# Optimization experiments

Measured on AMD Instinct MI355X. Metric: run time of the kernel, lower is better.

Reference implementation:

```python
import jax, jax.numpy as jnp
import numpy as np

N, E, EALL, C, R = 20000, 120000, 240000, 150, 1000
EH, RH, CH = 300, 100, 150


def _seg_softmax(e, idx, n):
    m = jax.ops.segment_max(e, idx, num_segments=n)
    ex = jnp.exp(e - m[idx])
    s = jax.ops.segment_sum(ex, idx, num_segments=n)
    return ex / s[idx]


def _l2norm(x):
    return x / jnp.clip(jnp.linalg.norm(x, axis=-1, keepdims=True), 1e-12, None)


def _highway(x1, x2, w, b):
    g = jax.nn.sigmoid(x1 @ w.T + b)
    return g * x2 + (1.0 - g) * x1


def _gcn(x, ei):
    n = x.shape[0]
    j, i = ei[0], ei[1]
    deg = jax.ops.segment_sum(jnp.ones(ei.shape[1], dtype=x.dtype), i, num_segments=n)
    dis = jnp.where(deg > 0, deg ** -0.5, 0.0)
    norm = dis[j] * dis[i]
    return jax.nn.relu(jax.ops.segment_sum(norm[:, None] * x[j], i, num_segments=n))


def _gat(x, ei, ai, aj):
    n = x.shape[0]
    j, i = ei[0], ei[1]
    e = (x @ ai)[i] + (x @ aj)[j]
    alpha = _seg_softmax(jax.nn.leaky_relu(e), i, n)
    return jax.nn.relu(jax.ops.segment_sum(alpha[:, None] * x[j], i, num_segments=n))


def _gat_e(x_e, im, io, rel, triple_num, r_emb, class_index, cls_ent,
           ac, ar, wh, wt, hww, hwb, main_is_head):
    n = x_e.shape[0]
    e_cnt = im.shape[0]
    c = cls_ent.shape[0]
    x_h = jax.nn.relu(x_e @ wh.T)
    x_t = jax.nn.relu(x_e @ wt.T)
    if main_is_head:
        x_m, x_o = x_h, x_t
        v1m, v2m, v3m = ac[0], ac[1], ac[2]
        v1o, v2o, v3o = ac[4], ac[5], ac[6]
    else:
        x_m, x_o = x_t, x_h
        v1m, v2m, v3m = ac[4], ac[5], ac[6]
        v1o, v2o, v3o = ac[0], ac[1], ac[2]
    v4, acv = ac[3], ac[7]
    e1 = 0.5 * ((x_m @ v1m)[im] + (x_o @ v1o)[io]) + (r_emb @ ar[0])[rel]
    alpha = _seg_softmax(jax.nn.leaky_relu(e1), triple_num, e_cnt)
    x_edge = _l2norm(x_m[im] * alpha[:, None])  # [E, c_hidden]
    e_r = 0.5 * ((r_emb @ ar[1])[rel] + 0.5 * ((x_edge @ v3m) + (x_o @ v3o)[io]))
    e = (x_o @ v2o)[io] + e_r + (x_edge @ v2m)
    beta = _seg_softmax(jax.nn.leaky_relu(e), class_index, c)
    # literal to source: the edge-level tensor is re-indexed by node ids in spmm
    x_class = jax.ops.segment_sum(beta[:, None] * x_edge[im], class_index, num_segments=c)
    e_c = (x_class @ acv) + (x_o @ v4)[cls_ent]
    gama = _seg_softmax(jax.nn.leaky_relu(e_c), cls_ent, n)
    out = jax.ops.segment_sum(gama[:, None] * x_class, cls_ent, num_segments=n)
    return _highway(x_o, out, hww, hwb)


def _forward(x_e, r_emb_table, hw1_w, hw1_b, hw2_w, hw2_b,
             h2r_ac, h2r_ar, h2r_wh, h2r_wt, h2r_hw_w, h2r_hw_b,
             et_ac, et_ar, et_wh, et_wt, et_hw_w, et_hw_b,
             gat_ai, gat_aj,
             edge_index, rel, edge_index_all, triple_num,
             class_index_head, head_class, class_index_tail, tail_class):
    r_emb = _l2norm(r_emb_table)
    x = _highway(x_e, _gcn(x_e, edge_index_all), hw1_w, hw1_b)
    x = _highway(x, _gcn(x, edge_index_all), hw2_w, hw2_b)
    eh, et = edge_index[0], edge_index[1]
    x_e_h = _gat_e(x, et, eh, rel, triple_num, r_emb, class_index_head, head_class,
                   h2r_ac, h2r_ar, h2r_wh, h2r_wt, h2r_hw_w, h2r_hw_b, False)
    x_e_t = _gat_e(x, eh, et, rel, triple_num, r_emb, class_index_tail, tail_class,
                   et_ac, et_ar, et_wh, et_wt, et_hw_w, et_hw_b, True)
    x1 = jnp.concatenate([x, x_e_h, x_e_t], axis=1)  # [N, 600]
    return jnp.concatenate([x, _gat(x1, edge_index_all, gat_ai, gat_aj)], axis=1)  # [N, 900]


def setup_inputs() -> dict:
    key = jax.random.key(0)
    ks = jax.random.split(key, 32)
    w = lambda k, shape: (jax.random.normal(k, shape, dtype=jnp.float32) * 0.05)
    return {
        'x_e': jax.random.normal(ks[0], (N, EH), dtype=jnp.float32),
        'edge_index': jax.random.randint(ks[1], (2, E), 0, N),
        'rel': jax.random.randint(ks[2], (E,), 0, R),
        'edge_index_all': jax.random.randint(ks[3], (2, EALL), 0, N),
        'triple_num': jax.random.randint(ks[4], (E,), 0, N),
        'class_index_head': jax.random.randint(ks[5], (E,), 0, C),
        'head_class': jax.random.randint(ks[6], (C,), 0, N),
        'class_index_tail': jax.random.randint(ks[7], (E,), 0, C),
        'tail_class': jax.random.randint(ks[8], (C,), 0, N),
        'r_emb_table': jax.random.normal(ks[9], (R, RH), dtype=jnp.float32),
        'hw1_w': w(ks[10], (EH, EH)), 'hw1_b': jnp.zeros((EH,), jnp.float32),
        'hw2_w': w(ks[11], (EH, EH)), 'hw2_b': jnp.zeros((EH,), jnp.float32),
        'h2r_ac': w(ks[12], (8, CH)), 'h2r_ar': w(ks[13], (2, RH)),
        'h2r_wh': w(ks[14], (CH, EH)), 'h2r_wt': w(ks[15], (CH, EH)),
        'h2r_hw_w': w(ks[16], (CH, CH)), 'h2r_hw_b': jnp.zeros((CH,), jnp.float32),
        'et_ac': w(ks[17], (8, CH)), 'et_ar': w(ks[18], (2, RH)),
        'et_wh': w(ks[19], (CH, EH)), 'et_wt': w(ks[20], (CH, EH)),
        'et_hw_w': w(ks[21], (CH, CH)), 'et_hw_b': jnp.zeros((CH,), jnp.float32),
        'gat_ai': w(ks[22], (2 * EH,)), 'gat_aj': w(ks[23], (2 * EH,)),
    }


def reference(x_e, edge_index, rel, edge_index_all, triple_num,
              class_index_head, head_class, class_index_tail, tail_class,
              r_emb_table, hw1_w, hw1_b, hw2_w, hw2_b,
              h2r_ac, h2r_ar, h2r_wh, h2r_wt, h2r_hw_w, h2r_hw_b,
              et_ac, et_ar, et_wh, et_wt, et_hw_w, et_hw_b,
              gat_ai, gat_aj):
    return _forward(x_e, r_emb_table, hw1_w, hw1_b, hw2_w, hw2_b,
                    h2r_ac, h2r_ar, h2r_wh, h2r_wt, h2r_hw_w, h2r_hw_b,
                    et_ac, et_ar, et_wh, et_wt, et_hw_w, et_hw_b,
                    gat_ai, gat_aj,
                    edge_index, rel, edge_index_all, triple_num,
                    class_index_head, head_class, class_index_tail, tail_class)
```

## Files before the change

### kernel.cpp

```cpp
#include <hip/hip_runtime.h>
#include <math.h>

#define Nn 20000
#define Ee 120000
#define EALLe 240000
#define Cc 150
#define Rr 1000
#define EHd 300
#define RHd 100
#define CHd 150
#define CB 128
#define XSPL 16

static inline int cdiv_h(int a, int b){ return (a + b - 1) / b; }

typedef __attribute__((ext_vector_type(8))) short short8;
typedef __attribute__((ext_vector_type(4))) float f32x4;

__device__ __forceinline__ float lrelu01(float x){ return x > 0.f ? x : 0.01f * x; }

__device__ __forceinline__ unsigned short f2b(float f){
  unsigned int u = __float_as_uint(f);
  unsigned int r = (u + 0x7FFFu + ((u >> 16) & 1u)) >> 16;
  return (unsigned short)r;
}
__device__ __forceinline__ float b2f(unsigned short u){
  return __uint_as_float(((unsigned int)u) << 16);
}
__device__ __forceinline__ float b2f_lo(unsigned int u){
  return __uint_as_float(u << 16);
}
__device__ __forceinline__ float b2f_hi(unsigned int u){
  return __uint_as_float(u & 0xFFFF0000u);
}

template<int Kq>
__device__ __forceinline__ void wredsumN(float* v){
#pragma unroll
  for (int m = 32; m >= 1; m >>= 1){
#pragma unroll
    for (int k = 0; k < Kq; k++) v[k] += __shfl_xor(v[k], m, 64);
  }
}

__global__ __launch_bounds__(64) void k_f2b(const float* __restrict__ src, int ncols,
    int ldsrc, unsigned short* __restrict__ dst, int ldp){
  int r = blockIdx.x, t = threadIdx.x;
  for (int c = t; c < ldp; c += 64)
    dst[(size_t)r * ldp + c] = (c < ncols) ? f2b(src[(size_t)r * ldsrc + c]) : (unsigned short)0;
}

struct Cvt8 {
  const float* s[8];
  unsigned short* d[8];
  int nc[8]; int lds[8]; int ldp[8]; int r0[9];
};
__global__ __launch_bounds__(64) void k_f2ball(Cvt8 c){
  int b = blockIdx.x, t = threadIdx.x;
  int idx = 0;
#pragma unroll
  for (int q = 1; q < 8; q++) if (b >= c.r0[q]) idx = q;
  int r = b - c.r0[idx];
  const float* src = c.s[idx] + (size_t)r * c.lds[idx];
  unsigned short* dst = c.d[idx] + (size_t)r * c.ldp[idx];
  int nc = c.nc[idx], ldp = c.ldp[idx];
  for (int col = t; col < ldp; col += 64)
    dst[col] = (col < nc) ? f2b(src[col]) : (unsigned short)0;
}

__global__ __launch_bounds__(64) void k_rnorm(const float* __restrict__ rt,
    const float* __restrict__ arh, const float* __restrict__ are,
    float* __restrict__ ra1h, float* __restrict__ ra1e){
  int r = blockIdx.x, lane = threadIdx.x;
  bool m1 = (lane + 64 < RHd);
  float v0 = rt[r * RHd + lane];
  float v1 = m1 ? rt[r * RHd + lane + 64] : 0.f;
  float s[3];
  s[0] = v0 * v0 + v1 * v1;
  s[1] = v0 * arh[RHd + lane] + (m1 ? v1 * arh[RHd + lane + 64] : 0.f);
  s[2] = v0 * are[RHd + lane] + (m1 ? v1 * are[RHd + lane + 64] : 0.f);
  wredsumN<3>(s);
  float inv = 0.5f / fmaxf(sqrtf(s[0]), 1e-12f);
  if (!lane){
    ra1h[r] = s[1] * inv;
    ra1e[r] = s[2] * inv;
  }
}

__global__ void k_count(const int* __restrict__ dst, int* __restrict__ degi){
  int e = blockIdx.x * blockDim.x + threadIdx.x;
  if (e < EALLe) atomicAdd(&degi[dst[e]], 1);
}

__global__ __launch_bounds__(1024) void k_scan(const int* __restrict__ degi,
    int* __restrict__ ptr, int* __restrict__ cur, float* __restrict__ dis){
  __shared__ int s[1024];
  int t = threadIdx.x;
  const int per = (Nn + 1023) / 1024;
  int b0 = t * per; if (b0 > Nn) b0 = Nn;
  int b1 = b0 + per; if (b1 > Nn) b1 = Nn;
  int sum = 0;
  for (int i = b0; i < b1; i++) sum += degi[i];
  s[t] = sum;
  __syncthreads();
  for (int off = 1; off < 1024; off <<= 1){
    int v = (t >= off) ? s[t - off] : 0;
    __syncthreads();
    s[t] += v;
    __syncthreads();
  }
  int run = (t > 0) ? s[t - 1] : 0;
  for (int i = b0; i < b1; i++){
    int dg = degi[i];
    ptr[i] = run; cur[i] = run; run += dg;
    dis[i] = dg > 0 ? rsqrtf((float)dg) : 0.f;
  }
  if (t == 1023) ptr[Nn] = s[1023];
}

__global__ void k_scatter(const int* __restrict__ src, const int* __restrict__ dst,
    int* __restrict__ cur, int* __restrict__ csr_src){
  int e = blockIdx.x * blockDim.x + threadIdx.x;
  if (e >= EALLe) return;
  int pos = atomicAdd(&cur[dst[e]], 1);
  csr_src[pos] = src[e];
}

__global__ __launch_bounds__(64) void k_gcnb(const unsigned short* __restrict__ x,
    const int* __restrict__ ptr, const int* __restrict__ src,
    const float* __restrict__ dis, float* __restrict__ out){
  int i = blockIdx.x, lane = threadIdx.x;
  int p0 = ptr[i], p1 = ptr[i + 1];
  float di = dis[i];
  bool m2 = lane < 22;
  float a0 = 0.f, a1 = 0.f, b0 = 0.f, b1 = 0.f, c0 = 0.f, c1 = 0.f;
  for (int k = p0; k < p1; k++){
    int j = src[k];
    float w = di * dis[j];
    const unsigned int* xr = (const unsigned int*)(x + (size_t)j * 320);
    unsigned int u0 = xr[lane];
    unsigned int u1 = xr[lane + 64];
    a0 += w * b2f_lo(u0); a1 += w * b2f_hi(u0);
    b0 += w * b2f_lo(u1); b1 += w * b2f_hi(u1);
    if (m2){
      unsigned int u2 = xr[lane + 128];
      c0 += w * b2f_lo(u2); c1 += w * b2f_hi(u2);
    }
  }
  float* orow = out + (size_t)i * EHd;
  orow[2 * lane]       = fmaxf(a0, 0.f);
  orow[2 * lane + 1]   = fmaxf(a1, 0.f);
  orow[128 + 2 * lane]     = fmaxf(b0, 0.f);
  orow[128 + 2 * lane + 1] = fmaxf(b1, 0.f);
  if (m2){
    orow[256 + 2 * lane]     = fmaxf(c0, 0.f);
    orow[256 + 2 * lane + 1] = fmaxf(c1, 0.f);
  }
}

__global__ __launch_bounds__(256) void k_gat3(const float* __restrict__ x1,
    const unsigned short* __restrict__ x1b,
    const int* __restrict__ ptr, const int* __restrict__ src,
    const float* __restrict__ s1, const float* __restrict__ s2,
    float* __restrict__ dout){
  __shared__ float wl[128];
  __shared__ int jl[128];
  int i = blockIdx.x, t = threadIdx.x;
  float* orow = dout + (size_t)i * 900;
  const float* xi = x1 + (size_t)i * 600;
  if (t < 75) ((f32x4*)orow)[t] = ((const f32x4*)xi)[t];
  int p0 = ptr[i], p1 = ptr[i + 1];
  if (p0 == p1){
    for (int f = t; f < 600; f += 256) orow[300 + f] = 0.f;
    return;
  }
  float s1i = s1[i];
  bool m2 = t < 44;
  float a0 = 0.f, a1 = 0.f, c0 = 0.f, c1 = 0.f, den = 0.f;
  for (int base = p0; base < p1; base += 128){
    int k = base + t;
    if (t < 128 && k < p1){
      int j = src[k];
      jl[t] = j;
      wl[t] = expf(lrelu01(s1i + s2[j]));
    }
    __syncthreads();
    int lim = p1 - base; if (lim > 128) lim = 128;
    for (int q = 0; q < lim; q++){
      float w = wl[q];
      den += w;
      const unsigned short* xj = x1b + (size_t)jl[q] * 600;
      unsigned int u = *(const unsigned int*)&xj[2 * t];
      a0 += w * b2f_lo(u);
      a1 += w * b2f_hi(u);
      if (m2){
        unsigned int v = *(const unsigned int*)&xj[512 + 2 * t];
        c0 += w * b2f_lo(v);
        c1 += w * b2f_hi(v);
      }
    }
    __syncthreads();
  }
  float invd = 1.f / den;
  orow[300 + 2 * t] = fmaxf(a0 * invd, 0.f);
  orow[300 + 2 * t + 1] = fmaxf(a1 * invd, 0.f);
  if (m2){
    orow[300 + 512 + 2 * t] = fmaxf(c0 * invd, 0.f);
    orow[300 + 512 + 2 * t + 1] = fmaxf(c1 * invd, 0.f);
  }
}

template<int EPI, int MIR>
__global__ __launch_bounds__(256) void k_gemmb(
    const unsigned short* __restrict__ Xb, int ldxb, int nrows,
    const unsigned short* __restrict__ Wb, int Kp, int M,
    const float* __restrict__ bias,
    const float* __restrict__ X2, int ldx2,
    const float* __restrict__ Xf, int ldxf,
    float* __restrict__ out, int ldo,
    unsigned short* __restrict__ mir, int ldmir){
  __shared__ unsigned short Xs[64][40];
  __shared__ unsigned short Ws[64][40];
  int t = threadIdx.x;
  int wv = t >> 6, lane = t & 63;
  int c0 = blockIdx.x * 64, r0 = blockIdx.y * 64;
  int srow = t >> 2, skoff = (t & 3) * 8;
  int gxr = r0 + srow, gwr = c0 + srow;
  f32x4 acc[4] = {};
  for (int k0 = 0; k0 < Kp; k0 += 32){
    short8 xv = {0,0,0,0,0,0,0,0};
    short8 wv8 = {0,0,0,0,0,0,0,0};
    if (gxr < nrows) xv = *(const short8*)&Xb[(size_t)gxr * ldxb + k0 + skoff];
    if (gwr < M)     wv8 = *(const short8*)&Wb[(size_t)gwr * Kp + k0 + skoff];
    __syncthreads();
    *(short8*)&Xs[srow][skoff] = xv;
    *(short8*)&Ws[srow][skoff] = wv8;
    __syncthreads();
    int arow = wv * 16 + (lane & 15);
    int kk = (lane >> 4) * 8;
    short8 af = *(const short8*)&Xs[arow][kk];
#pragma unroll
    for (int j = 0; j < 4; j++){
      short8 bf = *(const short8*)&Ws[j * 16 + (lane & 15)][kk];
      acc[j] = __builtin_amdgcn_mfma_f32_16x16x32_bf16(af, bf, acc[j], 0, 0, 0);
    }
  }
  int rbase = r0 + wv * 16 + (lane >> 4) * 4;
  int cbase = c0 + (lane & 15);
#pragma unroll
  for (int j = 0; j < 4; j++){
    int c = cbase + j * 16;
    if (c >= M) continue;
#pragma unroll
    for (int r = 0; r < 4; r++){
      int row = rbase + r;
      if (row >= nrows) continue;
      float v = acc[j][r];
      float o;
      if (EPI == 0){
        o = fmaxf(v, 0.f);
      } else {
        float g = 1.f / (1.f + expf(-(v + bias[c])));
        o = g * X2[(size_t)row * ldx2 + c] + (1.f - g) * Xf[(size_t)row * ldxf + c];
      }
      out[(size_t)row * ldo + c] = o;
      if (MIR) mir[(size_t)row * ldmir + c] = f2b(o);
    }
  }
}

__global__ __launch_bounds__(256) void k_hwgemm(
    const unsigned short* __restrict__ xob,
    const unsigned short* __restrict__ hwwbA, const unsigned short* __restrict__ hwwbB,
    const float* __restrict__ hwbA, const float* __restrict__ hwbB,
    const float* __restrict__ outb, const float* __restrict__ proj,
    float* __restrict__ x1, unsigned short* __restrict__ x1b){
  __shared__ unsigned short Xs[64][40];
  __shared__ unsigned short Ws[64][40];
  int g = blockIdx.z;
  const unsigned short* Xb = xob + (size_t)g * Nn * 160;
  const unsigned short* Wb = g ? hwwbB : hwwbA;
  const float* bias = g ? hwbB : hwbA;
  const float* X2 = outb + (size_t)g * Nn * CHd;
  const float* Xf = proj + (g ? 450 : 0);
  float* outp = x1 + (g ? 450 : 300);
  unsigned short* mir = x1b + (g ? 450 : 300);
  int t = threadIdx.x;
  int wv = t >> 6, lane = t & 63;
  int c0 = blockIdx.x * 64, r0 = blockIdx.y * 64;
  int srow = t >> 2, skoff = (t & 3) * 8;
  int gxr = r0 + srow, gwr = c0 + srow;
  f32x4 acc[4] = {};
  for (int k0 = 0; k0 < 160; k0 += 32){
    short8 xv = {0,0,0,0,0,0,0,0};
    short8 wv8 = {0,0,0,0,0,0,0,0};
    if (gxr < Nn) xv = *(const short8*)&Xb[(size_t)gxr * 160 + k0 + skoff];
    if (gwr < 150) wv8 = *(const short8*)&Wb[(size_t)gwr * 160 + k0 + skoff];
    __syncthreads();
    *(short8*)&Xs[srow][skoff] = xv;
    *(short8*)&Ws[srow][skoff] = wv8;
    __syncthreads();
    int arow = wv * 16 + (lane & 15);
    int kk = (lane >> 4) * 8;
    short8 af = *(const short8*)&Xs[arow][kk];
#pragma unroll
    for (int j = 0; j < 4; j++){
      short8 bf = *(const short8*)&Ws[j * 16 + (lane & 15)][kk];
      acc[j] = __builtin_amdgcn_mfma_f32_16x16x32_bf16(af, bf, acc[j], 0, 0, 0);
    }
  }
  int rbase = r0 + wv * 16 + (lane >> 4) * 4;
  int cbase = c0 + (lane & 15);
#pragma unroll
  for (int j = 0; j < 4; j++){
    int c = cbase + j * 16;
    if (c >= 150) continue;
#pragma unroll
    for (int r = 0; r < 4; r++){
      int row = rbase + r;
      if (row >= Nn) continue;
      float v = acc[j][r];
      float gg = 1.f / (1.f + expf(-(v + bias[c])));
      float o = gg * X2[(size_t)row * CHd + c] + (1.f - gg) * Xf[(size_t)row * 600 + c];
      outp[(size_t)row * 600 + c] = o;
      mir[(size_t)row * 600 + c] = f2b(o);
    }
  }
}

__global__ __launch_bounds__(64) void k_ndots2b(const float* __restrict__ proj,
    const float* __restrict__ h2r_ac, const float* __restrict__ et_ac,
    unsigned short* __restrict__ xob,
    unsigned short* __restrict__ xnb, float* __restrict__ pm,
    float* __restrict__ po, float* __restrict__ nv4){
  int n = blockIdx.x, g = blockIdx.y, lane = threadIdx.x;
  const float* ac = g ? et_ac : h2r_ac;
  const float* xm = proj + (g ? 300 : 150);
  const float* xo = proj + (g ? 450 : 0);
  const float* v2m = ac + (g ? 1 : 5) * CHd;
  const float* v2o = ac + (g ? 5 : 1) * CHd;
  const float* v3m = ac + (g ? 2 : 6) * CHd;
  const float* v3o = ac + (g ? 6 : 2) * CHd;
  const float* v4  = ac + 3 * CHd;
  bool m2 = lane < (CHd - 128);
  const float* mr = xm + (size_t)n * 600;
  const float* orw = xo + (size_t)n * 600;
  float m0 = mr[lane], m1 = mr[lane + 64], mv2 = m2 ? mr[lane + 128] : 0.f;
  float o0 = orw[lane], o1 = orw[lane + 64], o2 = m2 ? orw[lane + 128] : 0.f;
  unsigned short* xod = xob + (size_t)g * Nn * 160 + (size_t)n * 160;
  xod[lane] = f2b(o0);
  xod[lane + 64] = f2b(o1);
  if (m2) xod[lane + 128] = f2b(o2);
  if (lane < 10) xod[150 + lane] = 0;
  float s[4];
  s[0] = m0 * m0 + m1 * m1 + mv2 * mv2;
  s[1] = o0 * v2o[lane] + o1 * v2o[lane + 64] + (m2 ? o2 * v2o[lane + 128] : 0.f);
  s[2] = o0 * v3o[lane] + o1 * v3o[lane + 64] + (m2 ? o2 * v3o[lane + 128] : 0.f);
  s[3] = o0 * v4[lane]  + o1 * v4[lane + 64]  + (m2 ? o2 * v4[lane + 128]  : 0.f);
  wredsumN<4>(s);
  float inv = 1.f / fmaxf(sqrtf(s[0]), 1e-12f);
  float n0 = m0 * inv, n1 = m1 * inv, n2 = mv2 * inv;
  unsigned short* xr = xnb + (size_t)g * Nn * 152 + (size_t)n * 152;
  xr[lane] = f2b(n0); xr[lane + 64] = f2b(n1);
  if (m2) xr[lane + 128] = f2b(n2);
  float d[2];
  d[0] = n0 * v2m[lane] + n1 * v2m[lane + 64] + (m2 ? n2 * v2m[lane + 128] : 0.f);
  d[1] = n0 * v3m[lane] + n1 * v3m[lane + 64] + (m2 ? n2 * v3m[lane + 128] : 0.f);
  wredsumN<2>(d);
  if (!lane){
    pm[g * Nn + n] = d[0] + 0.25f * d[1];
    po[g * Nn + n] = s[1] + 0.25f * s[2];
    nv4[g * Nn + n] = s[3];
  }
}

__global__ __launch_bounds__(256) void k_e2sumb(const int* __restrict__ ei,
    const int* __restrict__ rel, const int* __restrict__ cih, const int* __restrict__ cit,
    const float* __restrict__ pm, const float* __restrict__ po,
    const float* __restrict__ ra1h, const float* __restrict__ ra1e,
    float* __restrict__ es2, float* __restrict__ csum_p, int* __restrict__ ccnt_p){
  __shared__ float ls[Cc];
  __shared__ int lc[Cc];
  int t = threadIdx.x, g = blockIdx.y;
  const int* im = ei + (g ? 0 : Ee);
  const int* io = ei + (g ? Ee : 0);
  const int* ci = g ? cit : cih;
  const float* ra1 = g ? ra1e : ra1h;
  const float* pmg = pm + g * Nn;
  const float* pog = po + g * Nn;
  float* es2g = es2 + (size_t)g * Ee;
  float* csg = csum_p + g * Cc * 16;
  int* ccg = ccnt_p + g * Cc * 16;
  for (int c = t; c < Cc; c += 256){ ls[c] = 0.f; lc[c] = 0; }
  __syncthreads();
  for (int e = blockIdx.x * 256 + t; e < Ee; e += gridDim.x * 256){
    float v = lrelu01(pog[io[e]] + pmg[im[e]] + ra1[rel[e]]);
    float s = expf(v);
    es2g[e] = s;
    int c = ci[e];
    atomicAdd(&ls[c], s);
    atomicAdd(&lc[c], 1);
  }
  __syncthreads();
  for (int c = t; c < Cc; c += 256){
    if (lc[c]){
      atomicAdd(&csg[c * 16], ls[c]);
      atomicAdd(&ccg[c * 16], lc[c]);
    }
  }
}

__global__ __launch_bounds__(256) void k_cscanb(const int* __restrict__ ccnt_p,
    int* __restrict__ cstart, int* __restrict__ ccur_p){
  __shared__ int s[Cc + 1];
  int t = threadIdx.x, g = blockIdx.x;
  const int* ccg = ccnt_p + g * Cc * 16;
  int* csg = cstart + g * (Cc + 1);
  int* cug = ccur_p + g * Cc * 16;
  if (t == 0){
    int run = 0;
    for (int c = 0; c < Cc; c++){ s[c] = run; run += ccg[c * 16]; }
    s[Cc] = run;
  }
  __syncthreads();
  if (t <= Cc) csg[t] = s[t];
  if (t < Cc) cug[t * 16] = s[t];
}

__global__ __launch_bounds__(256) void k_cscatterb(const int* __restrict__ ei,
    const int* __restrict__ cih, const int* __restrict__ cit,
    const float* __restrict__ es2,
    int* __restrict__ ccur_p, int* __restrict__ crows, float* __restrict__ cw){
  __shared__ int lcnt[Cc];
  __shared__ int lbase[Cc];
  int t = threadIdx.x, g = blockIdx.y;
  const int* im = ei + (g ? 0 : Ee);
  const int* ci = g ? cit : cih;
  const float* es2g = es2 + (size_t)g * Ee;
  int* cug = ccur_p + g * Cc * 16;
  int* crg = crows + (size_t)g * Ee;
  float* cwg = cw + (size_t)g * Ee;
  int epb = (Ee + gridDim.x - 1) / gridDim.x;
  int e0 = blockIdx.x * epb, e1 = e0 + epb; if (e1 > Ee) e1 = Ee;
  for (int c = t; c < Cc; c += 256) lcnt[c] = 0;
  __syncthreads();
  int myr[4], myc[4], mye[4]; int cnt = 0;
  for (int e = e0 + t; e < e1; e += 256){
    int c = ci[e];
    myr[cnt] = atomicAdd(&lcnt[c], 1);
    myc[cnt] = c; mye[cnt] = e; cnt++;
  }
  __syncthreads();
  for (int c = t; c < Cc; c += 256)
    lbase[c] = lcnt[c] ? atomicAdd(&cug[c * 16], lcnt[c]) : 0;
  __syncthreads();
  for (int q = 0; q < cnt; q++){
    int pos = lbase[myc[q]] + myr[q];
    int e = mye[q];
    crg[pos] = im[im[e]];
    cwg[pos] = es2g[e];
  }
}

__global__ __launch_bounds__(192) void k_xclassBb(
    const int* __restrict__ cstart, const int* __restrict__ crows,
    const float* __restrict__ cw, const float* __restrict__ csum_p,
    const unsigned short* __restrict__ xnb, float* __restrict__ x_class){
  int g = blockIdx.y;
  int c = blockIdx.x / XSPL, sp = blockIdx.x % XSPL;
  int t = threadIdx.x;
  const int* csg = cstart + g * (Cc + 1);
  const int* crg = crows + (size_t)g * Ee;
  const float* cwg = cw + (size_t)g * Ee;
  const unsigned short* xng = xnb + (size_t)g * Nn * 152;
  float* xcg = x_class + g * Cc * CHd;
  int p0 = csg[c], p1 = csg[c + 1];
  int len = p1 - p0;
  if (len <= 0) return;
  int chunk = (len + XSPL - 1) / XSPL;
  int q0 = p0 + sp * chunk;
  int q1 = q0 + chunk; if (q1 > p1) q1 = p1;
  if (q0 >= q1) return;
  bool act = t < CHd;
  float inv = 1.f / csum_p[g * Cc * 16 + c * 16];
  float acc = 0.f;
  int k = q0;
  for (; k + 4 <= q1; k += 4){
    int r0 = crg[k], r1 = crg[k + 1], r2 = crg[k + 2], r3 = crg[k + 3];
    float w0 = cwg[k] * inv, w1 = cwg[k + 1] * inv, w2 = cwg[k + 2] * inv, w3 = cwg[k + 3] * inv;
    if (act){
      acc += w0 * b2f(xng[(size_t)r0 * 152 + t]) + w1 * b2f(xng[(size_t)r1 * 152 + t])
           + w2 * b2f(xng[(size_t)r2 * 152 + t]) + w3 * b2f(xng[(size_t)r3 * 152 + t]);
    }
  }
  for (; k < q1; k++){
    if (act) acc += cwg[k] * inv * b2f(xng[(size_t)crg[k] * 152 + t]);
  }
  if (act) atomicAdd(&xcg[c * CHd + t], acc);
}

__global__ __launch_bounds__(256) void k_classfinalb(
    const float* __restrict__ x_class,
    const float* __restrict__ h2r_ac, const float* __restrict__ et_ac,
    const float* __restrict__ nv4,
    const int* __restrict__ hcls, const int* __restrict__ tcls,
    float* __restrict__ outb){
  __shared__ float v[Cc];
  __shared__ float gm[Cc];
  __shared__ int ce[Cc];
  int t = threadIdx.x, g = blockIdx.x;
  const float* xcg = x_class + g * Cc * CHd;
  const float* acv = (g ? et_ac : h2r_ac) + 7 * CHd;
  const float* nvg = nv4 + g * Nn;
  const int* cls_ent = g ? tcls : hcls;
  float* obg = outb + (size_t)g * Nn * CHd;
  if (t < Cc){
    ce[t] = cls_ent[t];
    float dot = 0.f;
    for (int f = 0; f < CHd; f++) dot += xcg[t * CHd + f] * acv[f];
    v[t] = lrelu01(dot + nvg[ce[t]]);
  }
  __syncthreads();
  if (t < Cc){
    int sgm = ce[t];
    float m = -3.0e38f;
    for (int c2 = 0; c2 < Cc; c2++) if (ce[c2] == sgm) m = fmaxf(m, v[c2]);
    float sum = 0.f;
    for (int c2 = 0; c2 < Cc; c2++) if (ce[c2] == sgm) sum += expf(v[c2] - m);
    gm[t] = expf(v[t] - m) / sum;
  }
  __syncthreads();
  for (int idx = t; idx < Cc * CHd; idx += 256){
    int c = idx / CHd, f = idx - c * CHd;
    atomicAdd(&obg[(size_t)ce[c] * CHd + f], gm[c] * xcg[c * CHd + f]);
  }
}

__global__ __launch_bounds__(64) void k_s12(const unsigned short* __restrict__ x1b,
    const float* __restrict__ ai, const float* __restrict__ aj,
    float* __restrict__ s1, float* __restrict__ s2){
  int n = blockIdx.x, lane = threadIdx.x;
  const unsigned int* xr = (const unsigned int*)(x1b + (size_t)n * 600);
  float sa = 0.f, sb = 0.f;
#pragma unroll
  for (int u = 0; u < 5; u++){
    int d = lane + u * 64;
    if (d < 300){
      unsigned int w = xr[d];
      float xlo = b2f_lo(w), xhi = b2f_hi(w);
      sa += xlo * ai[2 * d] + xhi * ai[2 * d + 1];
      sb += xlo * aj[2 * d] + xhi * aj[2 * d + 1];
    }
  }
  float s[2] = { sa, sb };
  wredsumN<2>(s);
  if (!lane){ s1[n] = s[0]; s2[n] = s[1]; }
}

extern "C" void kernel_launch(void* const* d_in, const int* in_sizes, int n_in,
                              void* d_out, int out_size, void* d_ws, size_t ws_size,
                              hipStream_t stream) {
  const float* x_e    = (const float*)d_in[0];
  const int*   ei     = (const int*)d_in[1];
  const int*   rel    = (const int*)d_in[2];
  const int*   eall   = (const int*)d_in[3];
  const int*   cih    = (const int*)d_in[5];
  const int*   hcls   = (const int*)d_in[6];
  const int*   cit    = (const int*)d_in[7];
  const int*   tcls   = (const int*)d_in[8];
  const float* remb   = (const float*)d_in[9];
  const float* hw1w   = (const float*)d_in[10];
  const float* hw1b   = (const float*)d_in[11];
  const float* hw2w   = (const float*)d_in[12];
  const float* hw2b   = (const float*)d_in[13];
  const float* h2r_ac = (const float*)d_in[14];
  const float* h2r_ar = (const float*)d_in[15];
  const float* h2r_wh = (const float*)d_in[16];
  const float* h2r_wt = (const float*)d_in[17];
  const float* h2r_hww= (const float*)d_in[18];
  const float* h2r_hwb= (const float*)d_in[19];
  const float* et_ac  = (const float*)d_in[20];
  const float* et_ar  = (const float*)d_in[21];
  const float* et_wh  = (const float*)d_in[22];
  const float* et_wt  = (const float*)d_in[23];
  const float* et_hww = (const float*)d_in[24];
  const float* et_hwb = (const float*)d_in[25];
  const float* gai    = (const float*)d_in[26];
  const float* gaj    = (const float*)d_in[27];
  float* out = (float*)d_out;

  char* wsp = (char*)d_ws;
  auto alloc = [&](size_t nbytes) -> void* {
    void* p = (void*)wsp;
    wsp += (nbytes + 255) & ~(size_t)255;
    return p;
  };
  float* ra1h = (float*)alloc(Rr * 4);
  float* ra1e = (float*)alloc(Rr * 4);
  float* dis  = (float*)alloc(Nn * 4);
  int* degi    = (int*)alloc(Nn * 4);
  int* csr_ptr = (int*)alloc((Nn + 1) * 4);
  int* csr_cur = (int*)alloc(Nn * 4);
  int* csr_src = (int*)alloc((size_t)EALLe * 4);
  float* x1  = (float*)alloc((size_t)Nn * 600 * 4);
  float* es2 = (float*)alloc((size_t)2 * Ee * 4);
  float* pm  = (float*)alloc(2 * Nn * 4);
  float* po  = (float*)alloc(2 * Nn * 4);
  float* nv4 = (float*)alloc(2 * Nn * 4);
  float* csum_p = (float*)alloc(2 * Cc * 16 * 4);
  int*   ccnt_p = (int*)alloc(2 * Cc * 16 * 4);
  float* x_class = (float*)alloc(2 * Cc * CHd * 4);
  size_t zregion = (size_t)((char*)x_class + ((2 * Cc * CHd * 4 + 255) & ~255)) - (size_t)(char*)csum_p;
  int*   ccur_p = (int*)alloc(2 * Cc * 16 * 4);
  int*   cstart = (int*)alloc(2 * (Cc + 1) * 4);
  int*   crows  = (int*)alloc((size_t)2 * Ee * 4);
  float* cw     = (float*)alloc((size_t)2 * Ee * 4);
  float* s1v = (float*)alloc(Nn * 4);
  float* s2v = (float*)alloc(Nn * 4);
  unsigned short* arenaA = (unsigned short*)alloc((size_t)Nn * 320 * 2);
  unsigned short* arenaB = (unsigned short*)alloc((size_t)Nn * 320 * 2);
  unsigned short* x1b    = (unsigned short*)alloc(((size_t)Nn * 600 + 64) * 2);
  unsigned short* w1b    = (unsigned short*)alloc((size_t)300 * 320 * 2);
  unsigned short* w2b    = (unsigned short*)alloc((size_t)300 * 320 * 2);
  unsigned short* wcatb  = (unsigned short*)alloc((size_t)600 * 320 * 2);
  unsigned short* hwwbA  = (unsigned short*)alloc((size_t)150 * 160 * 2);
  unsigned short* hwwbB  = (unsigned short*)alloc((size_t)150 * 160 * 2);
  unsigned short* xob = arenaA;
  unsigned short* xnb = arenaB;

  float* h1   = out;
  float* gbuf = out + (size_t)Nn * EHd;
  float* proj = out;
  float* outb = out + (size_t)Nn * 600;

  hipMemsetAsync(degi, 0, Nn * 4, stream);
  hipMemsetAsync(csum_p, 0, zregion, stream);
  hipMemsetAsync(outb, 0, (size_t)2 * Nn * CHd * 4, stream);
  k_rnorm<<<Rr, 64, 0, stream>>>(remb, h2r_ar, et_ar, ra1h, ra1e);
  k_count<<<cdiv_h(EALLe, 256), 256, 0, stream>>>(eall + EALLe, degi);
  k_scan<<<1, 1024, 0, stream>>>(degi, csr_ptr, csr_cur, dis);
  k_scatter<<<cdiv_h(EALLe, 256), 256, 0, stream>>>(eall, eall + EALLe, csr_cur, csr_src);
  {
    Cvt8 cv;
    cv.s[0] = hw1w;    cv.d[0] = w1b;                         cv.nc[0] = 300; cv.lds[0] = 300; cv.ldp[0] = 320;
    cv.s[1] = hw2w;    cv.d[1] = w2b;                         cv.nc[1] = 300; cv.lds[1] = 300; cv.ldp[1] = 320;
    cv.s[2] = h2r_wh;  cv.d[2] = wcatb + (size_t)0   * 320;   cv.nc[2] = 300; cv.lds[2] = 300; cv.ldp[2] = 320;
    cv.s[3] = h2r_wt;  cv.d[3] = wcatb + (size_t)150 * 320;   cv.nc[3] = 300; cv.lds[3] = 300; cv.ldp[3] = 320;
    cv.s[4] = et_wh;   cv.d[4] = wcatb + (size_t)300 * 320;   cv.nc[4] = 300; cv.lds[4] = 300; cv.ldp[4] = 320;
    cv.s[5] = et_wt;   cv.d[5] = wcatb + (size_t)450 * 320;   cv.nc[5] = 300; cv.lds[5] = 300; cv.ldp[5] = 320;
    cv.s[6] = h2r_hww; cv.d[6] = hwwbA;                       cv.nc[6] = 150; cv.lds[6] = 150; cv.ldp[6] = 160;
    cv.s[7] = et_hww;  cv.d[7] = hwwbB;                       cv.nc[7] = 150; cv.lds[7] = 150; cv.ldp[7] = 160;
    cv.r0[0] = 0;    cv.r0[1] = 300;  cv.r0[2] = 600;  cv.r0[3] = 750;
    cv.r0[4] = 900;  cv.r0[5] = 1050; cv.r0[6] = 1200; cv.r0[7] = 1350; cv.r0[8] = 1500;
    k_f2ball<<<1500, 64, 0, stream>>>(cv);
  }
  k_f2b<<<Nn, 64, 0, stream>>>(x_e, 300, 300, arenaA, 320);

  k_gcnb<<<Nn, 64, 0, stream>>>(arenaA, csr_ptr, csr_src, dis, gbuf);
  k_gemmb<1,1><<<dim3(5, cdiv_h(Nn, 64)), 256, 0, stream>>>(
      arenaA, 320, Nn, w1b, 320, 300, hw1b, gbuf, 300, x_e, 300, h1, 300, arenaB, 320);
  k_gcnb<<<Nn, 64, 0, stream>>>(arenaB, csr_ptr, csr_src, dis, gbuf);
  k_gemmb<1,1><<<dim3(5, cdiv_h(Nn, 64)), 256, 0, stream>>>(
      arenaB, 320, Nn, w2b, 320, 300, hw2b, gbuf, 300, h1, 300, x1, 600, x1b, 600);

  k_gemmb<0,0><<<dim3(10, cdiv_h(Nn, 64)), 256, 0, stream>>>(
      x1b, 600, Nn, wcatb, 320, 600, nullptr, nullptr, 0, nullptr, 0, proj, 600,
      nullptr, 0);

  k_ndots2b<<<dim3(Nn, 2), 64, 0, stream>>>(proj, h2r_ac, et_ac, xob, xnb, pm, po, nv4);
  k_e2sumb<<<dim3(CB, 2), 256, 0, stream>>>(ei, rel, cih, cit, pm, po, ra1h, ra1e,
                                            es2, csum_p, ccnt_p);
  k_cscanb<<<2, 256, 0, stream>>>(ccnt_p, cstart, ccur_p);
  k_cscatterb<<<dim3(CB, 2), 256, 0, stream>>>(ei, cih, cit, es2, ccur_p, crows, cw);
  k_xclassBb<<<dim3(Cc * XSPL, 2), 192, 0, stream>>>(cstart, crows, cw, csum_p,
                                                     xnb, x_class);
  k_classfinalb<<<2, 256, 0, stream>>>(x_class, h2r_ac, et_ac, nv4, hcls, tcls, outb);
  k_hwgemm<<<dim3(3, cdiv_h(Nn, 64), 2), 256, 0, stream>>>(
      xob, hwwbA, hwwbB, h2r_hwb, et_hwb, outb, proj, x1, x1b);

  k_s12<<<Nn, 64, 0, stream>>>(x1b, gai, gaj, s1v, s2v);
  k_gat3<<<Nn, 256, 0, stream>>>(x1, x1b, csr_ptr, csr_src, s1v, s2v, out);
}
```

Baseline: 525.7 us.

## Split neighbor loop across thread groups with 16-byte loads in GCN and GAT aggregation

```diff
diff --git a/kernel.cpp b/kernel.cpp
--- a/kernel.cpp
+++ b/kernel.cpp
@@ -126,45 +126,80 @@
   csr_src[pos] = src[e];
 }
 
-__global__ __launch_bounds__(64) void k_gcnb(const unsigned short* __restrict__ x,
+__global__ __launch_bounds__(256) void k_gcn4(const unsigned short* __restrict__ x,
     const int* __restrict__ ptr, const int* __restrict__ src,
     const float* __restrict__ dis, float* __restrict__ out){
-  int i = blockIdx.x, lane = threadIdx.x;
+  __shared__ float wl[128];
+  __shared__ int jl[128];
+  __shared__ float red[5][40][8];
+  int i = blockIdx.x, t = threadIdx.x;
   int p0 = ptr[i], p1 = ptr[i + 1];
+  float* orow = out + (size_t)i * 300;
+  if (p0 == p1){
+    for (int f = t; f < 300; f += 256) orow[f] = 0.f;
+    return;
+  }
+  int g = t / 40, c = t - g * 40;
+  bool act = t < 240;
   float di = dis[i];
-  bool m2 = lane < 22;
-  float a0 = 0.f, a1 = 0.f, b0 = 0.f, b1 = 0.f, c0 = 0.f, c1 = 0.f;
-  for (int k = p0; k < p1; k++){
-    int j = src[k];
-    float w = di * dis[j];
-    const unsigned int* xr = (const unsigned int*)(x + (size_t)j * 320);
-    unsigned int u0 = xr[lane];
-    unsigned int u1 = xr[lane + 64];
-    a0 += w * b2f_lo(u0); a1 += w * b2f_hi(u0);
-    b0 += w * b2f_lo(u1); b1 += w * b2f_hi(u1);
-    if (m2){
-      unsigned int u2 = xr[lane + 128];
-      c0 += w * b2f_lo(u2); c1 += w * b2f_hi(u2);
-    }
-  }
-  float* orow = out + (size_t)i * EHd;
-  orow[2 * lane]       = fmaxf(a0, 0.f);
-  orow[2 * lane + 1]   = fmaxf(a1, 0.f);
-  orow[128 + 2 * lane]     = fmaxf(b0, 0.f);
-  orow[128 + 2 * lane + 1] = fmaxf(b1, 0.f);
-  if (m2){
-    orow[256 + 2 * lane]     = fmaxf(c0, 0.f);
-    orow[256 + 2 * lane + 1] = fmaxf(c1, 0.f);
-  }
-}
-
-__global__ __launch_bounds__(256) void k_gat3(const float* __restrict__ x1,
+  float acc[8] = {};
+  for (int base = p0; base < p1; base += 128){
+    int k = base + t;
+    if (t < 128 && k < p1){
+      int j = src[k];
+      jl[t] = j;
+      wl[t] = di * dis[j];
+    }
+    __syncthreads();
+    int lim = p1 - base; if (lim > 128) lim = 128;
+    if (act){
+      for (int q = g; q < lim; q += 6){
+        float w = wl[q];
+        const unsigned short* xr = x + (size_t)jl[q] * 320;
+        union { f32x4 f; unsigned int u[4]; } U;
+        U.f = *(const f32x4*)&xr[8 * c];
+#pragma unroll
+        for (int h = 0; h < 4; h++){
+          acc[2 * h]     += w * b2f_lo(U.u[h]);
+          acc[2 * h + 1] += w * b2f_hi(U.u[h]);
+        }
+      }
+    }
+    __syncthreads();
+  }
+  if (act && g > 0){
+#pragma unroll
+    for (int h = 0; h < 8; h++) red[g - 1][c][h] = acc[h];
+  }
+  __syncthreads();
+  if (g == 0){
+#pragma unroll
+    for (int h = 0; h < 8; h++){
+      float v = acc[h];
+#pragma unroll
+      for (int r = 0; r < 5; r++) v += red[r][c][h];
+      acc[h] = fmaxf(v, 0.f);
+    }
+    int col0 = 8 * c;
+    if (col0 + 8 <= 300){
+      f32x4 o0 = { acc[0], acc[1], acc[2], acc[3] };
+      f32x4 o1 = { acc[4], acc[5], acc[6], acc[7] };
+      *(f32x4*)&orow[col0] = o0;
+      *(f32x4*)&orow[col0 + 4] = o1;
+    } else {
+      for (int h = 0; h < 8 && col0 + h < 300; h++) orow[col0 + h] = acc[h];
+    }
+  }
+}
+
+__global__ __launch_bounds__(256) void k_gat4(const float* __restrict__ x1,
     const unsigned short* __restrict__ x1b,
     const int* __restrict__ ptr, const int* __restrict__ src,
     const float* __restrict__ s1, const float* __restrict__ s2,
     float* __restrict__ dout){
   __shared__ float wl[128];
   __shared__ int jl[128];
+  __shared__ float red[2][75][8];
   int i = blockIdx.x, t = threadIdx.x;
   float* orow = dout + (size_t)i * 900;
   const float* xi = x1 + (size_t)i * 600;
@@ -175,8 +210,10 @@
     return;
   }
   float s1i = s1[i];
-  bool m2 = t < 44;
-  float a0 = 0.f, a1 = 0.f, c0 = 0.f, c1 = 0.f, den = 0.f;
+  int g = t / 75, c = t - g * 75;
+  bool act = t < 225;
+  float acc[8] = {};
+  float den = 0.f;
   for (int base = p0; base < p1; base += 128){
     int k = base + t;
     if (t < 128 && k < p1){
@@ -186,27 +223,38 @@
     }
     __syncthreads();
     int lim = p1 - base; if (lim > 128) lim = 128;
-    for (int q = 0; q < lim; q++){
-      float w = wl[q];
-      den += w;
-      const unsigned short* xj = x1b + (size_t)jl[q] * 600;
-      unsigned int u = *(const unsigned int*)&xj[2 * t];
-      a0 += w * b2f_lo(u);
-      a1 += w * b2f_hi(u);
-      if (m2){
-        unsigned int v = *(const unsigned int*)&xj[512 + 2 * t];
-        c0 += w * b2f_lo(v);
-        c1 += w * b2f_hi(v);
+    for (int q = 0; q < lim; q++) den += wl[q];
+    if (act){
+      for (int q = g; q < lim; q += 3){
+        float w = wl[q];
+        const unsigned short* xj = x1b + (size_t)jl[q] * 600;
+        union { f32x4 f; unsigned int u[4]; } U;
+        U.f = *(const f32x4*)&xj[8 * c];
+#pragma unroll
+        for (int h = 0; h < 4; h++){
+          acc[2 * h]     += w * b2f_lo(U.u[h]);
+          acc[2 * h + 1] += w * b2f_hi(U.u[h]);
+        }
       }
     }
     __syncthreads();
   }
-  float invd = 1.f / den;
-  orow[300 + 2 * t] = fmaxf(a0 * invd, 0.f);
-  orow[300 + 2 * t + 1] = fmaxf(a1 * invd, 0.f);
-  if (m2){
-    orow[300 + 512 + 2 * t] = fmaxf(c0 * invd, 0.f);
-    orow[300 + 512 + 2 * t + 1] = fmaxf(c1 * invd, 0.f);
+  if (act && g > 0){
+#pragma unroll
+    for (int h = 0; h < 8; h++) red[g - 1][c][h] = acc[h];
+  }
+  __syncthreads();
+  if (g == 0){
+    float invd = 1.f / den;
+#pragma unroll
+    for (int h = 0; h < 8; h++){
+      float v = acc[h] + red[0][c][h] + red[1][c][h];
+      acc[h] = fmaxf(v * invd, 0.f);
+    }
+    f32x4 o0 = { acc[0], acc[1], acc[2], acc[3] };
+    f32x4 o1 = { acc[4], acc[5], acc[6], acc[7] };
+    ((f32x4*)(orow + 300))[2 * c] = o0;
+    ((f32x4*)(orow + 300))[2 * c + 1] = o1;
   }
 }
 
@@ -656,10 +704,10 @@
   }
   k_f2b<<<Nn, 64, 0, stream>>>(x_e, 300, 300, arenaA, 320);
 
-  k_gcnb<<<Nn, 64, 0, stream>>>(arenaA, csr_ptr, csr_src, dis, gbuf);
+  k_gcn4<<<Nn, 256, 0, stream>>>(arenaA, csr_ptr, csr_src, dis, gbuf);
   k_gemmb<1,1><<<dim3(5, cdiv_h(Nn, 64)), 256, 0, stream>>>(
       arenaA, 320, Nn, w1b, 320, 300, hw1b, gbuf, 300, x_e, 300, h1, 300, arenaB, 320);
-  k_gcnb<<<Nn, 64, 0, stream>>>(arenaB, csr_ptr, csr_src, dis, gbuf);
+  k_gcn4<<<Nn, 256, 0, stream>>>(arenaB, csr_ptr, csr_src, dis, gbuf);
   k_gemmb<1,1><<<dim3(5, cdiv_h(Nn, 64)), 256, 0, stream>>>(
       arenaB, 320, Nn, w2b, 320, 300, hw2b, gbuf, 300, h1, 300, x1, 600, x1b, 600);
 
@@ -679,5 +727,5 @@
       xob, hwwbA, hwwbB, h2r_hwb, et_hwb, outb, proj, x1, x1b);
 
   k_s12<<<Nn, 64, 0, stream>>>(x1b, gai, gaj, s1v, s2v);
-  k_gat3<<<Nn, 256, 0, stream>>>(x1, x1b, csr_ptr, csr_src, s1v, s2v, out);
-}
+  k_gat4<<<Nn, 256, 0, stream>>>(x1, x1b, csr_ptr, csr_src, s1v, s2v, out);
+}
```

New measurement: 511.7 us. 1.03x faster.
